# Kernel tuning notes

Measured on AMD Instinct MI355X. Metric: run time of the kernel, lower is better.

Reference implementation:

```python
import jax, jax.numpy as jnp
import numpy as np

B, S, D, E, K = 2, 2048, 512, 8, 2
H = 4 * D  # 2048


def setup_inputs() -> dict:
    key = jax.random.key(0)
    ks = jax.random.split(key, 6)
    x = jax.random.normal(ks[0], (B, S, D), dtype=jnp.float32)
    # parameters, matching torch init (randn weights, zero biases)
    w1 = jax.random.normal(ks[1], (E, D, H), dtype=jnp.float32)
    w2 = jax.random.normal(ks[2], (E, H, D), dtype=jnp.float32)
    b1 = jnp.zeros((E, H), dtype=jnp.float32)
    b2 = jnp.zeros((E, D), dtype=jnp.float32)
    # nn.Linear(D, E): kaiming-uniform-ish; plain uniform is fine for a baseline
    lim = 1.0 / np.sqrt(D)
    router_w = jax.random.uniform(ks[3], (D, E), dtype=jnp.float32, minval=-lim, maxval=lim)
    router_b = jax.random.uniform(ks[4], (E,), dtype=jnp.float32, minval=-lim, maxval=lim)
    return {"x": x, "w1": w1, "w2": w2, "b1": b1, "b2": b2,
            "router_w": router_w, "router_b": router_b}


def reference(x, w1, w2, b1, b2, router_w, router_b):
    # router: [b,s,e]
    router_logits = jnp.einsum('bsd,de->bse', x, router_w) + router_b
    top_k_logits, top_k_indices = jax.lax.top_k(router_logits, K)   # [b,s,k]
    top_k_probs = jax.nn.softmax(top_k_logits, axis=-1)             # [b,s,k]
    masks = jax.nn.one_hot(top_k_indices, E, dtype=x.dtype)          # [b,s,k,e]
    # dense all-expert MLP (faithful to source: every expert on every token)
    h = jnp.einsum('bsd,edh->bseh', x, w1) + b1                      # [b,s,e,4d]
    h = jax.nn.gelu(h, approximate=False)                            # exact gelu
    y = jnp.einsum('bseh,ehd->bsed', h, w2) + b2                     # [b,s,e,d]
    # combine: mask each expert output by routed prob and sum over top-k
    out = jnp.einsum('bsed,bske,bsk->bsd', y, masks, top_k_probs)    # [b,s,d]
    return out
```

## Files before the change

### kernel.cpp

```cpp
#include <hip/hip_runtime.h>
#include <math.h>

typedef unsigned short u16;
typedef __bf16 bf16x8 __attribute__((ext_vector_type(8)));
typedef float f32x4 __attribute__((ext_vector_type(4)));

#define T_TOKENS 4096
#define D_DIM    512
#define H_DIM    2048
#define E_NUM    8
#define CAP      4096
#define NSLOT    (T_TOKENS * 2)

__device__ __forceinline__ u16 f2bf(float f) {
  unsigned int u = __builtin_bit_cast(unsigned int, f);
  u = (u + 0x7fffu + ((u >> 16) & 1u)) >> 16;
  return (u16)u;
}

__device__ __forceinline__ void gload16(const void* g, void* l) {
  __builtin_amdgcn_global_load_lds(
      (__attribute__((address_space(1))) void*)(g),
      (__attribute__((address_space(3))) void*)(l), 16, 0, 0);
}

__device__ __forceinline__ float gelu_fast(float v) {
  float u = v * __fmaf_rn(0.071354817f, v * v, 1.59576912f);
  return v / (1.0f + __expf(-u));
}

__global__ __launch_bounds__(256) void transpose_bf16_kernel(const float* __restrict__ in,
                                                             u16* __restrict__ out,
                                                             int R, int C) {
  __shared__ float tile[32][33];
  const int e = blockIdx.z;
  const int c0 = blockIdx.x * 32, r0 = blockIdx.y * 32;
  const float* src = in + (size_t)e * R * C;
  u16* dst = out + (size_t)e * R * C;
  const int tx = threadIdx.x, ty = threadIdx.y;
#pragma unroll
  for (int i = 0; i < 4; i++)
    tile[ty + 8 * i][tx] = src[(size_t)(r0 + ty + 8 * i) * C + c0 + tx];
  __syncthreads();
#pragma unroll
  for (int i = 0; i < 4; i++)
    dst[(size_t)(c0 + ty + 8 * i) * R + r0 + tx] = f2bf(tile[tx][ty + 8 * i]);
}

__global__ __launch_bounds__(256) void router_kernel(const float* __restrict__ x,
                                                     const float* __restrict__ rw,
                                                     const float* __restrict__ rb,
                                                     int* __restrict__ topk_idx,
                                                     float* __restrict__ topk_p,
                                                     u16* __restrict__ xb) {
  const int lane = threadIdx.x & 63;
  const int t = blockIdx.x * 4 + (threadIdx.x >> 6);
  const float* xr = x + (size_t)t * D_DIM + lane * 8;
  float xv[8];
  *(float4*)(&xv[0]) = *(const float4*)(xr);
  *(float4*)(&xv[4]) = *(const float4*)(xr + 4);
  ushort4 o0, o1;
  o0.x = f2bf(xv[0]); o0.y = f2bf(xv[1]); o0.z = f2bf(xv[2]); o0.w = f2bf(xv[3]);
  o1.x = f2bf(xv[4]); o1.y = f2bf(xv[5]); o1.z = f2bf(xv[6]); o1.w = f2bf(xv[7]);
  ushort4* xo = (ushort4*)(xb + (size_t)t * D_DIM + lane * 8);
  xo[0] = o0; xo[1] = o1;

  float acc[8] = {0.f,0.f,0.f,0.f,0.f,0.f,0.f,0.f};
#pragma unroll
  for (int j = 0; j < 8; j++) {
    const float4* w = (const float4*)(rw + (size_t)(lane * 8 + j) * E_NUM);
    float4 w0 = w[0], w1 = w[1];
    acc[0] += xv[j] * w0.x; acc[1] += xv[j] * w0.y;
    acc[2] += xv[j] * w0.z; acc[3] += xv[j] * w0.w;
    acc[4] += xv[j] * w1.x; acc[5] += xv[j] * w1.y;
    acc[6] += xv[j] * w1.z; acc[7] += xv[j] * w1.w;
  }
#pragma unroll
  for (int off = 32; off > 0; off >>= 1) {
#pragma unroll
    for (int e = 0; e < 8; e++) acc[e] += __shfl_down(acc[e], off);
  }
  if (lane == 0) {
    float l[8];
#pragma unroll
    for (int e = 0; e < 8; e++) l[e] = acc[e] + rb[e];
    int i0 = 0; float v0 = l[0];
#pragma unroll
    for (int e = 1; e < 8; e++) if (l[e] > v0) { v0 = l[e]; i0 = e; }
    int i1 = -1; float v1 = -3.4e38f;
#pragma unroll
    for (int e = 0; e < 8; e++) if (e != i0 && l[e] > v1) { v1 = l[e]; i1 = e; }
    float p1 = expf(v1 - v0);
    float s = 1.0f + p1;
    topk_idx[t * 2] = i0; topk_idx[t * 2 + 1] = i1;
    topk_p[t * 2] = 1.0f / s; topk_p[t * 2 + 1] = p1 / s;
  }
}

__global__ __launch_bounds__(256) void compact_kernel(const int* __restrict__ topk_idx,
                                                      const float* __restrict__ topk_p,
                                                      int* __restrict__ slot_list,
                                                      float* __restrict__ prob_list,
                                                      int* __restrict__ counts) {
  const int e = blockIdx.x;
  const int tid = threadIdx.x, lane = tid & 63, w = tid >> 6;
  __shared__ int wsum[4];
  __shared__ int sbase;
  if (tid == 0) sbase = 0;
  __syncthreads();
  for (int c0 = 0; c0 < T_TOKENS; c0 += 256) {
    const int t = c0 + tid;
    const int i0 = topk_idx[t * 2], i1 = topk_idx[t * 2 + 1];
    int flag = 0, slot = 0; float p = 0.f;
    if (i0 == e)      { flag = 1; slot = t * 2;     p = topk_p[t * 2]; }
    else if (i1 == e) { flag = 1; slot = t * 2 + 1; p = topk_p[t * 2 + 1]; }
    unsigned long long m = __ballot(flag);
    if (lane == 0) wsum[w] = (int)__popcll(m);
    const int wpre = (int)__popcll(m & ((1ull << lane) - 1ull));
    __syncthreads();
    int base = sbase;
#pragma unroll
    for (int j = 0; j < 4; j++) if (j < w) base += wsum[j];
    const int tot = wsum[0] + wsum[1] + wsum[2] + wsum[3];
    if (flag) { slot_list[e * CAP + base + wpre] = slot; prob_list[e * CAP + base + wpre] = p; }
    __syncthreads();
    if (tid == 0) sbase += tot;
  }
  __syncthreads();
  if (tid == 0) counts[e] = sbase;
}

__global__ __launch_bounds__(256) void gemm1_kernel(const u16* __restrict__ xb,
                                                    const u16* __restrict__ w1t,
                                                    const float* __restrict__ b1,
                                                    const int* __restrict__ slot_list,
                                                    const float* __restrict__ prob_list,
                                                    const int* __restrict__ counts,
                                                    u16* __restrict__ hbuf) {
  const int e  = blockIdx.y >> 5;
  const int rt = blockIdx.y & 31;
  const int cnt = counts[e];
  const int rbase = rt * 128;
  if (rbase >= cnt) return;
  const int n0 = blockIdx.x * 128;

  __shared__ __align__(16) u16 At[2][128 * 64];
  __shared__ __align__(16) u16 Bt[2][128 * 64];

  const int tid = threadIdx.x, lane = tid & 63, wid = tid >> 6;
  const int wr = wid >> 1, wc = wid & 1;
  const int lr8 = lane >> 3;
  const int sx = lane & 7;
  const int kperm = (sx ^ lr8) * 8;
  const int lrow = lane & 15, lk = lane >> 4;

  const u16* pa[4]; const u16* pb[4]; int lo[4];
#pragma unroll
  for (int i = 0; i < 4; i++) {
    const int row = (wid * 4 + i) * 8 + lr8;
    const int grow = rbase + row;
    int tok = 0;
    if (grow < cnt) tok = slot_list[e * CAP + grow] >> 1;
    pa[i] = xb + (size_t)tok * D_DIM + kperm;
    pb[i] = w1t + ((size_t)e * H_DIM + n0 + row) * D_DIM + kperm;
    lo[i] = (wid * 4 + i) * 512;
  }

  f32x4 acc[4][4];
#pragma unroll
  for (int i = 0; i < 4; i++)
#pragma unroll
    for (int j = 0; j < 4; j++) acc[i][j] = (f32x4){0.f, 0.f, 0.f, 0.f};

  auto stage = [&](int k0, int b) {
#pragma unroll
    for (int i = 0; i < 4; i++) gload16(pa[i] + k0, &At[b][lo[i]]);
#pragma unroll
    for (int i = 0; i < 4; i++) gload16(pb[i] + k0, &Bt[b][lo[i]]);
  };

  stage(0, 0);
  __syncthreads();
  int cur = 0;
  const int nt = D_DIM / 64;
  for (int t = 0; t < nt; ++t) {
    if (t + 1 < nt) stage((t + 1) * 64, cur ^ 1);
#pragma unroll
    for (int ks = 0; ks < 2; ks++) {
      bf16x8 afr[4], bfr[4];
#pragma unroll
      for (int f = 0; f < 4; f++) {
        afr[f] = *(const bf16x8*)(&At[cur][(wr * 64 + f * 16 + lrow) * 64 + ((ks * 4 + lk) ^ sx) * 8]);
        bfr[f] = *(const bf16x8*)(&Bt[cur][(wc * 64 + f * 16 + lrow) * 64 + ((ks * 4 + lk) ^ sx) * 8]);
      }
#pragma unroll
      for (int fr = 0; fr < 4; fr++)
#pragma unroll
        for (int fc = 0; fc < 4; fc++)
          acc[fr][fc] = __builtin_amdgcn_mfma_f32_16x16x32_bf16(afr[fr], bfr[fc], acc[fr][fc], 0, 0, 0);
    }
    __syncthreads();
    cur ^= 1;
  }

  float bias[4];
#pragma unroll
  for (int fc = 0; fc < 4; fc++) bias[fc] = b1[e * H_DIM + n0 + wc * 64 + fc * 16 + lrow];
#pragma unroll
  for (int fr = 0; fr < 4; fr++) {
#pragma unroll
    for (int reg = 0; reg < 4; reg++) {
      const int rloc = wr * 64 + fr * 16 + lk * 4 + reg;
      const int grow = rbase + rloc;
      if (grow < cnt) {
        const int slot = slot_list[e * CAP + grow];
        const float p  = prob_list[e * CAP + grow];
        u16* dst = hbuf + (size_t)slot * H_DIM + n0 + wc * 64 + lrow;
#pragma unroll
        for (int fc = 0; fc < 4; fc++) {
          float v = acc[fr][fc][reg] + bias[fc];
          dst[fc * 16] = f2bf(gelu_fast(v) * p);
        }
      }
    }
  }
}

__global__ __launch_bounds__(256) void gemm2_kernel(const u16* __restrict__ hbuf,
                                                    const u16* __restrict__ w2t,
                                                    const float* __restrict__ b2,
                                                    const int* __restrict__ slot_list,
                                                    const float* __restrict__ prob_list,
                                                    const int* __restrict__ counts,
                                                    float* __restrict__ ypart) {
  const int e  = blockIdx.y >> 6;
  const int rt = blockIdx.y & 63;
  const int s  = blockIdx.z;
  const int cnt = counts[e];
  const int rbase = rt * 64;
  if (rbase >= cnt) return;
  const int n0 = blockIdx.x * 128;
  const int kb = s * (H_DIM / 2);

  __shared__ __align__(16) u16 At[2][64 * 64];
  __shared__ __align__(16) u16 Bt[2][128 * 64];

  const int tid = threadIdx.x, lane = tid & 63, wid = tid >> 6;
  const int wr = wid >> 1, wc = wid & 1;
  const int lr8 = lane >> 3;
  const int sx = lane & 7;
  const int kperm = (sx ^ lr8) * 8;
  const int lrow = lane & 15, lk = lane >> 4;

  const u16* pa[2]; int loa[2];
#pragma unroll
  for (int i = 0; i < 2; i++) {
    const int row = (wid * 2 + i) * 8 + lr8;
    const int grow = rbase + row;
    int slot = 0;
    if (grow < cnt) slot = slot_list[e * CAP + grow];
    pa[i] = hbuf + (size_t)slot * H_DIM + kb + kperm;
    loa[i] = (wid * 2 + i) * 512;
  }
  const u16* pb[4]; int lob[4];
#pragma unroll
  for (int i = 0; i < 4; i++) {
    const int row = (wid * 4 + i) * 8 + lr8;
    pb[i] = w2t + ((size_t)e * D_DIM + n0 + row) * H_DIM + kb + kperm;
    lob[i] = (wid * 4 + i) * 512;
  }

  f32x4 acc[2][4];
#pragma unroll
  for (int i = 0; i < 2; i++)
#pragma unroll
    for (int j = 0; j < 4; j++) acc[i][j] = (f32x4){0.f, 0.f, 0.f, 0.f};

  auto stage = [&](int k0, int b) {
#pragma unroll
    for (int i = 0; i < 2; i++) gload16(pa[i] + k0, &At[b][loa[i]]);
#pragma unroll
    for (int i = 0; i < 4; i++) gload16(pb[i] + k0, &Bt[b][lob[i]]);
  };

  stage(0, 0);
  __syncthreads();
  int cur = 0;
  const int nt = (H_DIM / 2) / 64;
  for (int t = 0; t < nt; ++t) {
    if (t + 1 < nt) stage((t + 1) * 64, cur ^ 1);
#pragma unroll
    for (int ks = 0; ks < 2; ks++) {
      bf16x8 afr[2], bfr[4];
#pragma unroll
      for (int f = 0; f < 2; f++)
        afr[f] = *(const bf16x8*)(&At[cur][(wr * 32 + f * 16 + lrow) * 64 + ((ks * 4 + lk) ^ sx) * 8]);
#pragma unroll
      for (int f = 0; f < 4; f++)
        bfr[f] = *(const bf16x8*)(&Bt[cur][(wc * 64 + f * 16 + lrow) * 64 + ((ks * 4 + lk) ^ sx) * 8]);
#pragma unroll
      for (int fr = 0; fr < 2; fr++)
#pragma unroll
        for (int fc = 0; fc < 4; fc++)
          acc[fr][fc] = __builtin_amdgcn_mfma_f32_16x16x32_bf16(afr[fr], bfr[fc], acc[fr][fc], 0, 0, 0);
    }
    __syncthreads();
    cur ^= 1;
  }

#pragma unroll
  for (int fr = 0; fr < 2; fr++) {
#pragma unroll
    for (int reg = 0; reg < 4; reg++) {
      const int rloc = wr * 32 + fr * 16 + lk * 4 + reg;
      const int grow = rbase + rloc;
      if (grow < cnt) {
        const int slot = slot_list[e * CAP + grow];
        const float p  = prob_list[e * CAP + grow];
        float* dst = ypart + ((size_t)s * NSLOT + slot) * D_DIM + n0 + wc * 64 + lrow;
#pragma unroll
        for (int fc = 0; fc < 4; fc++) {
          float v = acc[fr][fc][reg];
          if (s == 0) v += p * b2[e * D_DIM + n0 + wc * 64 + fc * 16 + lrow];
          dst[fc * 16] = v;
        }
      }
    }
  }
}

__global__ __launch_bounds__(256) void combine_kernel(const float* __restrict__ yp,
                                                      float* __restrict__ out) {
  int i = blockIdx.x * 256 + threadIdx.x;
  int t = i >> 7;
  int dq = i & 127;
  float4 a = ((const float4*)(yp + (size_t)(t * 2) * D_DIM))[dq];
  float4 b = ((const float4*)(yp + (size_t)(t * 2 + 1) * D_DIM))[dq];
  float4 c = ((const float4*)(yp + ((size_t)NSLOT + t * 2) * D_DIM))[dq];
  float4 d = ((const float4*)(yp + ((size_t)NSLOT + t * 2 + 1) * D_DIM))[dq];
  float4 r;
  r.x = a.x + b.x + c.x + d.x;
  r.y = a.y + b.y + c.y + d.y;
  r.z = a.z + b.z + c.z + d.z;
  r.w = a.w + b.w + c.w + d.w;
  ((float4*)(out + (size_t)t * D_DIM))[dq] = r;
}

extern "C" void kernel_launch(void* const* d_in, const int* in_sizes, int n_in,
                              void* d_out, int out_size, void* d_ws, size_t ws_size,
                              hipStream_t stream) {
  const float* x  = (const float*)d_in[0];
  const float* w1 = (const float*)d_in[1];
  const float* w2 = (const float*)d_in[2];
  const float* b1 = (const float*)d_in[3];
  const float* b2 = (const float*)d_in[4];
  const float* rw = (const float*)d_in[5];
  const float* rb = (const float*)d_in[6];
  float* out = (float*)d_out;

  char* ws = (char*)d_ws;
  size_t off = 0;
  auto alloc = [&](size_t bytes) -> void* {
    void* p = ws + off;
    off = (off + bytes + 255) & ~(size_t)255;
    return p;
  };
  int*   counts    = (int*)alloc(E_NUM * 4);
  int*   slot_list = (int*)alloc((size_t)E_NUM * CAP * 4);
  float* prob_list = (float*)alloc((size_t)E_NUM * CAP * 4);
  int*   topk_idx  = (int*)alloc((size_t)T_TOKENS * 2 * 4);
  float* topk_p    = (float*)alloc((size_t)T_TOKENS * 2 * 4);
  u16*   xb        = (u16*)alloc((size_t)T_TOKENS * D_DIM * 2);
  u16*   w1t       = (u16*)alloc((size_t)E_NUM * H_DIM * D_DIM * 2);
  u16*   w2t       = (u16*)alloc((size_t)E_NUM * H_DIM * D_DIM * 2);
  u16*   hbuf      = (u16*)alloc((size_t)NSLOT * H_DIM * 2);
  float* ypart     = (float*)alloc((size_t)2 * NSLOT * D_DIM * 4);

  transpose_bf16_kernel<<<dim3(H_DIM / 32, D_DIM / 32, E_NUM), dim3(32, 8), 0, stream>>>(w1, w1t, D_DIM, H_DIM);
  transpose_bf16_kernel<<<dim3(D_DIM / 32, H_DIM / 32, E_NUM), dim3(32, 8), 0, stream>>>(w2, w2t, H_DIM, D_DIM);
  router_kernel<<<T_TOKENS / 4, 256, 0, stream>>>(x, rw, rb, topk_idx, topk_p, xb);
  compact_kernel<<<E_NUM, 256, 0, stream>>>(topk_idx, topk_p, slot_list, prob_list, counts);
  gemm1_kernel<<<dim3(H_DIM / 128, E_NUM * 32), 256, 0, stream>>>(xb, w1t, b1, slot_list, prob_list, counts, hbuf);
  gemm2_kernel<<<dim3(D_DIM / 128, E_NUM * 64, 2), 256, 0, stream>>>(hbuf, w2t, b2, slot_list, prob_list, counts, ypart);
  combine_kernel<<<(T_TOKENS * D_DIM / 4) / 256, 256, 0, stream>>>(ypart, out);
}
```

Measured before the change: 145.2 us.

## Prefetch two K-tiles ahead in expert GEMMs and vectorize weight transpose

Both expert GEMM kernels now issue global-to-LDS loads two tiles ahead. They wait on vmcnt and use split barriers so the next tile's loads overlap the current tile's MFMAs, and they raise wave priority around the MFMA block. All LDS fragments for a tile are read into registers before the buffer is released for refill. The fp32-to-bf16 weight transpose uses 64x64 tiles with float4 loads and 16-byte stores to cut per-element memory transactions. The hand-written vmcnt counts depend on how many loads each stage issues, so a mismatch would cause races. The stray label in the transpose is harmless but odd.

```diff
diff --git a/kernel.cpp b/kernel.cpp
--- a/kernel.cpp
+++ b/kernel.cpp
@@ -32,19 +32,32 @@
 __global__ __launch_bounds__(256) void transpose_bf16_kernel(const float* __restrict__ in,
                                                              u16* __restrict__ out,
                                                              int R, int C) {
-  __shared__ float tile[32][33];
+  __shared__ float tile[64][67];
   const int e = blockIdx.z;
-  const int c0 = blockIdx.x * 32, r0 = blockIdx.y * 32;
+  const int c0 = blockIdx.x * 64, r0 = blockIdx.y * 64;
   const float* src = in + (size_t)e * R * C;
   u16* dst = out + (size_t)e * R * C;
-  const int tx = threadIdx.x, ty = threadIdx.y;
-#pragma unroll
-  for (int i = 0; i < 4; i++)
-    tile[ty + 8 * i][tx] = src[(size_t)(r0 + ty + 8 * i) * C + c0 + tx];
+  const int tid = threadIdx.x;
+  {
+    const int row = tid >> 2, cc = (tid & 3) * 16;
+    const float* s = src + (size_t)(r0 + row) * C + c0 + cc;
+#pragma unroll
+    for (int j = 0; j < 4; j++) {
+      float4 v = *(const float4*)(s + 4 * j);
+      *(float4*)(&tile[row][cc + 4 * j]) = v;
+    }
+  }
   __syncthreads();
-#pragma unroll
-  for (int i = 0; i < 4; i++)
-    dst[(size_t)(c0 + ty + 8 * i) * R + r0 + tx] = f2bf(tile[tx][ty + 8 * i]);
+  {
+    const int c = tid >> 2, rc = (tid & 3) * 16;
+    ushort8_t: ;
+    u16 buf[16];
+#pragma unroll
+    for (int j = 0; j < 16; j++) buf[j] = f2bf(tile[rc + j][c]);
+    u16* d = dst + (size_t)(c0 + c) * R + r0 + rc;
+    *(uint4*)(d) = *(uint4*)(&buf[0]);
+    *(uint4*)(d + 8) = *(uint4*)(&buf[8]);
+  }
 }
 
 __global__ __launch_bounds__(256) void router_kernel(const float* __restrict__ x,
@@ -180,27 +193,37 @@
   };
 
   stage(0, 0);
-  __syncthreads();
-  int cur = 0;
+  stage(64, 1);
   const int nt = D_DIM / 64;
+#pragma unroll
   for (int t = 0; t < nt; ++t) {
-    if (t + 1 < nt) stage((t + 1) * 64, cur ^ 1);
-#pragma unroll
-    for (int ks = 0; ks < 2; ks++) {
-      bf16x8 afr[4], bfr[4];
+    const int cur = t & 1;
+    if (t < nt - 1) { asm volatile("s_waitcnt vmcnt(8)" ::: "memory"); }
+    else            { asm volatile("s_waitcnt vmcnt(0)" ::: "memory"); }
+    __builtin_amdgcn_sched_barrier(0);
+    __builtin_amdgcn_s_barrier();
+    bf16x8 afr[4][2], bfr[4][2];
+#pragma unroll
+    for (int ks = 0; ks < 2; ks++)
 #pragma unroll
       for (int f = 0; f < 4; f++) {
-        afr[f] = *(const bf16x8*)(&At[cur][(wr * 64 + f * 16 + lrow) * 64 + ((ks * 4 + lk) ^ sx) * 8]);
-        bfr[f] = *(const bf16x8*)(&Bt[cur][(wc * 64 + f * 16 + lrow) * 64 + ((ks * 4 + lk) ^ sx) * 8]);
+        afr[f][ks] = *(const bf16x8*)(&At[cur][(wr * 64 + f * 16 + lrow) * 64 + ((ks * 4 + lk) ^ sx) * 8]);
+        bfr[f][ks] = *(const bf16x8*)(&Bt[cur][(wc * 64 + f * 16 + lrow) * 64 + ((ks * 4 + lk) ^ sx) * 8]);
       }
+    asm volatile("s_waitcnt lgkmcnt(0)" ::: "memory");
+    __builtin_amdgcn_sched_barrier(0);
+    __builtin_amdgcn_s_barrier();
+    if (t + 2 < nt) stage((t + 2) * 64, cur);
+    __builtin_amdgcn_sched_barrier(0);
+    __builtin_amdgcn_s_setprio(1);
+#pragma unroll
+    for (int ks = 0; ks < 2; ks++)
 #pragma unroll
       for (int fr = 0; fr < 4; fr++)
 #pragma unroll
         for (int fc = 0; fc < 4; fc++)
-          acc[fr][fc] = __builtin_amdgcn_mfma_f32_16x16x32_bf16(afr[fr], bfr[fc], acc[fr][fc], 0, 0, 0);
-    }
-    __syncthreads();
-    cur ^= 1;
+          acc[fr][fc] = __builtin_amdgcn_mfma_f32_16x16x32_bf16(afr[fr][ks], bfr[fc][ks], acc[fr][fc], 0, 0, 0);
+    __builtin_amdgcn_s_setprio(0);
   }
 
   float bias[4];
@@ -284,28 +307,39 @@
   };
 
   stage(0, 0);
-  __syncthreads();
-  int cur = 0;
+  stage(64, 1);
   const int nt = (H_DIM / 2) / 64;
+#pragma unroll
   for (int t = 0; t < nt; ++t) {
-    if (t + 1 < nt) stage((t + 1) * 64, cur ^ 1);
+    const int cur = t & 1;
+    if (t < nt - 1) { asm volatile("s_waitcnt vmcnt(6)" ::: "memory"); }
+    else            { asm volatile("s_waitcnt vmcnt(0)" ::: "memory"); }
+    __builtin_amdgcn_sched_barrier(0);
+    __builtin_amdgcn_s_barrier();
+    bf16x8 afr[2][2], bfr[4][2];
 #pragma unroll
     for (int ks = 0; ks < 2; ks++) {
-      bf16x8 afr[2], bfr[4];
 #pragma unroll
       for (int f = 0; f < 2; f++)
-        afr[f] = *(const bf16x8*)(&At[cur][(wr * 32 + f * 16 + lrow) * 64 + ((ks * 4 + lk) ^ sx) * 8]);
+        afr[f][ks] = *(const bf16x8*)(&At[cur][(wr * 32 + f * 16 + lrow) * 64 + ((ks * 4 + lk) ^ sx) * 8]);
 #pragma unroll
       for (int f = 0; f < 4; f++)
-        bfr[f] = *(const bf16x8*)(&Bt[cur][(wc * 64 + f * 16 + lrow) * 64 + ((ks * 4 + lk) ^ sx) * 8]);
+        bfr[f][ks] = *(const bf16x8*)(&Bt[cur][(wc * 64 + f * 16 + lrow) * 64 + ((ks * 4 + lk) ^ sx) * 8]);
+    }
+    asm volatile("s_waitcnt lgkmcnt(0)" ::: "memory");
+    __builtin_amdgcn_sched_barrier(0);
+    __builtin_amdgcn_s_barrier();
+    if (t + 2 < nt) stage((t + 2) * 64, cur);
+    __builtin_amdgcn_sched_barrier(0);
+    __builtin_amdgcn_s_setprio(1);
+#pragma unroll
+    for (int ks = 0; ks < 2; ks++)
 #pragma unroll
       for (int fr = 0; fr < 2; fr++)
 #pragma unroll
         for (int fc = 0; fc < 4; fc++)
-          acc[fr][fc] = __builtin_amdgcn_mfma_f32_16x16x32_bf16(afr[fr], bfr[fc], acc[fr][fc], 0, 0, 0);
-    }
-    __syncthreads();
-    cur ^= 1;
+          acc[fr][fc] = __builtin_amdgcn_mfma_f32_16x16x32_bf16(afr[fr][ks], bfr[fc][ks], acc[fr][fc], 0, 0, 0);
+    __builtin_amdgcn_s_setprio(0);
   }
 
 #pragma unroll
@@ -376,8 +410,8 @@
   u16*   hbuf      = (u16*)alloc((size_t)NSLOT * H_DIM * 2);
   float* ypart     = (float*)alloc((size_t)2 * NSLOT * D_DIM * 4);
 
-  transpose_bf16_kernel<<<dim3(H_DIM / 32, D_DIM / 32, E_NUM), dim3(32, 8), 0, stream>>>(w1, w1t, D_DIM, H_DIM);
-  transpose_bf16_kernel<<<dim3(D_DIM / 32, H_DIM / 32, E_NUM), dim3(32, 8), 0, stream>>>(w2, w2t, H_DIM, D_DIM);
+  transpose_bf16_kernel<<<dim3(H_DIM / 64, D_DIM / 64, E_NUM), 256, 0, stream>>>(w1, w1t, D_DIM, H_DIM);
+  transpose_bf16_kernel<<<dim3(D_DIM / 64, H_DIM / 64, E_NUM), 256, 0, stream>>>(w2, w2t, H_DIM, D_DIM);
   router_kernel<<<T_TOKENS / 4, 256, 0, stream>>>(x, rw, rb, topk_idx, topk_p, xb);
   compact_kernel<<<E_NUM, 256, 0, stream>>>(topk_idx, topk_p, slot_list, prob_list, counts);
   gemm1_kernel<<<dim3(H_DIM / 128, E_NUM * 32), 256, 0, stream>>>(xb, w1t, b1, slot_list, prob_list, counts, hbuf);
```

Result: faster. 136.3 us (-6.2%).
